# Optimization experiments

Hardware: AMD Instinct MI355X
Metric: run time of the kernel (lower is better)

The kernel has to match this reference:

```python
import jax, jax.numpy as jnp
import numpy as np

B, L, K = 16, 512, 30          # proteins, residues per protein, kNN neighbors
N = B * L
H, FC = 32, 3                  # h_channels, frame_channels
C = H + FC                     # fused sphere channels (35)
HEADS, AC, VC = 8, 16, 8       # heads, alpha channels (H//2), value channels (H//4)
RBF_N, POS_N = 16, 16
EF = RBF_N + POS_N

# idealized backbone atom positions (N, CA, C) in the local residue frame
IDEAL_BB = np.array([[-0.525, 1.363, 0.0], [0.0, 0.0, 0.0], [1.526, 0.0, 0.0]], dtype=np.float32)
# cartesian (x,y,z) -> real-SH l=1 ordering (y,z,x)
P_SH = np.array([[0., 1., 0.], [0., 0., 1.], [1., 0., 0.]], dtype=np.float32)


def _knn_edges(trans):
    # per-chain brute-force kNN (chains are contiguous blocks of length L)
    X = trans.reshape(B, L, 3)
    d2 = jnp.sum((X[:, :, None, :] - X[:, None, :, :]) ** 2, axis=-1)  # [B,L,L]
    d2 = d2 + jnp.eye(L, dtype=d2.dtype) * 1e9                          # exclude self
    _, idx = jax.lax.top_k(-d2, K)                                      # [B,L,K]
    off = (jnp.arange(B) * L)[:, None, None]
    src = (idx + off).reshape(-1)              # neighbor (edge_index[0])
    tgt = jnp.repeat(jnp.arange(N), K)         # center   (edge_index[1])
    return src, tgt


def _edge_rot_mat(vec):
    # rotation aligning the edge vector with the y axis (eSCN init_edge_rot_mat style)
    nx = vec / (jnp.linalg.norm(vec, axis=-1, keepdims=True) + 1e-12)
    ref = jnp.where(jnp.abs(nx[:, :1]) < 0.9,
                    jnp.array([1., 0., 0.], dtype=vec.dtype),
                    jnp.array([0., 0., 1.], dtype=vec.dtype))
    nz = jnp.cross(nx, ref)
    nz = nz / (jnp.linalg.norm(nz, axis=-1, keepdims=True) + 1e-12)
    ny = jnp.cross(nx, nz)
    ny = ny / (jnp.linalg.norm(ny, axis=-1, keepdims=True) + 1e-12)
    return jnp.stack([nz, nx, ny], axis=-2)  # [E,3,3]


def _rbf(d, d_min=0.0, d_max=20.0, count=RBF_N):
    mu = jnp.linspace(d_min, d_max, count)
    sigma = (d_max - d_min) / count
    return jnp.exp(-(((d[:, None] - mu) / sigma) ** 2))


def _pos_emb(src, tgt, num=POS_N):
    d = (src - tgt).astype(jnp.float32)
    freq = jnp.exp(jnp.arange(0, num, 2, dtype=jnp.float32) * (-np.log(10000.0) / num))
    ang = d[:, None] * freq
    return jnp.concatenate([jnp.cos(ang), jnp.sin(ang)], axis=-1)


def _forward(rots, trans, node_emb, batch, x_mask, noising_mask,
             W_alpha, a_vec, W_v, W_o, W_g, W_2):
    src, tgt = _knn_edges(trans)
    vec = trans[src] - trans[tgt]
    dist = jnp.linalg.norm(vec, axis=-1)
    valid = jnp.isfinite(dist) & (dist > 1e-3)  # edge_select, applied as mask

    R = _edge_rot_mat(vec)
    P = jnp.asarray(P_SH)
    D1 = jnp.einsum('ij,ejk,lk->eil', P, R, P)  # l=1 Wigner in real-SH basis [E,3,3]

    edge_features = jnp.concatenate([_rbf(dist), _pos_emb(src, tgt)], axis=-1)  # [E,32]

    # fuse node features with backbone frame atoms and editability flag
    frame_atoms = jnp.einsum('nij,aj->nai', rots, jnp.asarray(IDEAL_BB))  # [N,3atoms,3xyz]
    editable = noising_mask & (~x_mask)
    emb = jnp.zeros((N, 4, C), dtype=node_emb.dtype)
    emb = emb.at[:, :, :H].set(node_emb)
    emb = emb.at[:, 1:4, H:].set(jnp.swapaxes(frame_atoms, -1, -2))
    emb = emb.at[:, 0, C - 1].set(editable.astype(node_emb.dtype))

    # gather + rotate source features into edge frames
    xs = emb[src]                                                   # [E,4,C]
    xs_rot = jnp.concatenate([xs[:, :1], jnp.einsum('eij,ejc->eic', D1, xs[:, 1:])], axis=1)

    # invariant attention logits (l=0 of rotated src, l=0 of tgt, edge feats)
    inv = jnp.concatenate([xs_rot[:, 0], emb[tgt, 0], edge_features], axis=-1)  # [E,102]
    hdn = jax.nn.silu(inv @ W_alpha).reshape(-1, HEADS, AC)
    logits = jax.nn.leaky_relu(jnp.einsum('ehk,hk->eh', hdn, a_vec), 0.2)
    logits = jnp.where(valid[:, None], logits, -1e9)

    # segment softmax over incoming edges of each target node
    mx = jax.lax.stop_gradient(jax.ops.segment_max(logits, tgt, num_segments=N))
    ex = jnp.exp(logits - mx[tgt]) * valid[:, None].astype(logits.dtype)
    den = jax.ops.segment_sum(ex, tgt, num_segments=N)
    alpha = ex / (den[tgt] + 1e-9)                                  # [E,HEADS]

    # equivariant values, attention-weighted, rotate back, scatter
    v = (xs_rot @ W_v).reshape(-1, 4, HEADS, VC)
    m = (v * alpha[:, None, :, None]).reshape(-1, 4, HEADS * VC)
    m = jnp.concatenate([m[:, :1], jnp.einsum('eji,ejc->eic', D1, m[:, 1:])], axis=1)  # D^T
    agg = jax.ops.segment_sum(m, tgt, num_segments=N)               # [N,4,64]

    y = agg @ W_o                                                    # [N,4,H]
    gate = jax.nn.silu(y[:, 0] @ W_g)                                # invariant gating FFN
    return (y * gate[:, None, :]) @ W_2                              # [N,4,H]


def setup_inputs():
    key = jax.random.key(0)
    ks = jax.random.split(key, 12)
    rots = jax.vmap(lambda m: jnp.linalg.qr(m)[0])(jax.random.normal(ks[0], (N, 3, 3)))
    trans = jax.random.normal(ks[1], (N, 3)) * 10.0
    node_emb = jax.random.normal(ks[2], (N, 4, H))
    batch = jnp.repeat(jnp.arange(B, dtype=jnp.int32), L)
    x_mask = jax.random.randint(ks[3], (N,), 0, 2).astype(bool)
    noising_mask = jax.random.randint(ks[4], (N,), 0, 2).astype(bool)
    s = lambda k, sh, fan: jax.random.normal(k, sh) / np.sqrt(fan)
    return dict(rots=rots, trans=trans, node_emb=node_emb, batch=batch,
                x_mask=x_mask, noising_mask=noising_mask,
                W_alpha=s(ks[5], (2 * C + EF, HEADS * AC), 2 * C + EF),
                a_vec=s(ks[6], (HEADS, AC), AC),
                W_v=s(ks[7], (C, HEADS * VC), C),
                W_o=s(ks[8], (HEADS * VC, H), HEADS * VC),
                W_g=s(ks[9], (H, H), H),
                W_2=s(ks[10], (H, H), H))


def reference(rots, trans, node_emb, batch, x_mask, noising_mask,
              W_alpha, a_vec, W_v, W_o, W_g, W_2):
    return _forward(rots, trans, node_emb, batch, x_mask, noising_mask,
                    W_alpha, a_vec, W_v, W_o, W_g, W_2)
```

## Files before the change

### kernel.cpp

```cpp
#include <hip/hip_runtime.h>
#include <cstdint>

#define B_ 16
#define L_ 512
#define N_ 8192
#define K_ 30
#define E_ (N_*K_)
#define H_ 32
#define C_ 35

typedef uint16_t u16;
typedef uint32_t u32;
typedef unsigned long long u64;
typedef float f2v __attribute__((ext_vector_type(2)));

static __device__ __forceinline__ f2v splat2(float x) { f2v v; v.x = x; v.y = x; return v; }

static __device__ __forceinline__ float ldf(const void* p, int i, int bf) {
    return bf ? __uint_as_float(((u32)((const u16*)p)[i]) << 16)
              : ((const float*)p)[i];
}
static __device__ __forceinline__ float bfu16(u16 x) {
    return __uint_as_float(((u32)x) << 16);
}
static __device__ __forceinline__ int ldmask(const void* p, int i, int mode) {
    if (mode == 0) return ((const unsigned char*)p)[i] != 0;
    if (mode == 2) return ((const u32*)p)[2*i] != 0;
    return ((const u32*)p)[i] != 0;
}
static __device__ __forceinline__ u16 f2bf(float f) {
    u32 x = __float_as_uint(f);
    u32 r = x + 0x7FFFu + ((x >> 16) & 1u);
    return (u16)(r >> 16);
}
static __device__ __forceinline__ float fsilu(float x) {
    return x * __builtin_amdgcn_rcpf(1.f + __expf(-x));
}

static __device__ __forceinline__ int detect_bf(const void* tr, int lane) {
    const u16* p = (const u16*)tr;
    int cnt = 0;
    for (int i = lane; i < 256; i += 64) {
        u16 v = p[2 * i];
        int e = (v >> 7) & 0xFF;
        if ((e >= 100 && e <= 141) || (v & 0x7FFFu) == 0) cnt++;
    }
    #pragma unroll
    for (int d = 1; d < 64; d <<= 1) cnt += __shfl_xor(cnt, d, 64);
    return cnt >= 192;
}
static __device__ __forceinline__ int detect_mm(const void* xmv, int lane) {
    const u32* xm = (const u32*)xmv;
    int anyBig = 0, oddNZ = 0;
    for (int i = lane; i < 1024; i += 64) {
        u32 w = xm[i];
        if (w & ~1u) anyBig = 1;
        if ((i & 1) && w) oddNZ = 1;
    }
    #pragma unroll
    for (int d = 1; d < 64; d <<= 1) {
        anyBig |= __shfl_xor(anyBig, d, 64);
        oddNZ  |= __shfl_xor(oddNZ, d, 64);
    }
    return anyBig ? 0 : (oddNZ ? 1 : 2);
}

__constant__ float cBB[9] = {-0.525f, 1.363f, 0.f,  0.f, 0.f, 0.f,  1.526f, 0.f, 0.f};

#define DPP_UMIN(var, CTRL) \
    { u32 o_ = (u32)__builtin_amdgcn_update_dpp((int)(var), (int)(var), CTRL, 0xF, 0xF, false); \
      (var) = (o_ < (var)) ? o_ : (var); }
#define DPP_UMIN_ALL(var) \
    DPP_UMIN(var, 0x111) DPP_UMIN(var, 0x112) DPP_UMIN(var, 0x114) \
    DPP_UMIN(var, 0x118) DPP_UMIN(var, 0x142) DPP_UMIN(var, 0x143)

__global__ __launch_bounds__(256) void mega_kernel(
    const void* __restrict__ rots, const void* __restrict__ trans,
    const void* __restrict__ node, const void* __restrict__ xm,
    const void* __restrict__ nm,
    const void* __restrict__ Wa, const void* __restrict__ av,
    const void* __restrict__ Wv, const void* __restrict__ Wo,
    const void* __restrict__ Wg, const void* __restrict__ W2,
    int* __restrict__ flag, int* __restrict__ srcArr,
    float* __restrict__ hsrc, float* __restrict__ htgt,
    float* __restrict__ ptab, float* __restrict__ V,
    float* __restrict__ c_wrb, float* __restrict__ c_av,
    float* __restrict__ c_Wo, float* __restrict__ c_Wg, float* __restrict__ c_W2)
{
    __shared__ float sX[L_], sY[L_], sZ[L_];
    __shared__ float eS[140];
    __shared__ int flagS[2];
    const int bid = blockIdx.x, tid = threadIdx.x;
    const int lane = tid & 63, wid = tid >> 6;

    if (bid < 2048) {
        if (wid == 0) {
            int bf = detect_bf(trans, lane);
            if (lane == 0) flagS[0] = bf;
        }
        __syncthreads();
        const int bf = flagS[0];
        const int t0 = bid * 4;
        const int base = (t0 >> 9) << 9;
        if (bf) {
            const u16* tp = (const u16*)trans;
            for (int i = tid; i < L_; i += 256) {
                sX[i] = bfu16(tp[(base + i) * 3 + 0]);
                sY[i] = bfu16(tp[(base + i) * 3 + 1]);
                sZ[i] = bfu16(tp[(base + i) * 3 + 2]);
            }
        } else {
            const float* tp = (const float*)trans;
            for (int i = tid; i < L_; i += 256) {
                sX[i] = tp[(base + i) * 3 + 0];
                sY[i] = tp[(base + i) * 3 + 1];
                sZ[i] = tp[(base + i) * 3 + 2];
            }
        }
        __syncthreads();

        const int t = t0 + wid;
        const int l = t & 511;
        const float tx = sX[l], ty = sY[l], tz = sZ[l];

        u32 d2b[8];
        #pragma unroll
        for (int i = 0; i < 8; ++i) {
            int j = lane + (i << 6);
            float dx = __fsub_rn(tx, sX[j]);
            float dy = __fsub_rn(ty, sY[j]);
            float dz = __fsub_rn(tz, sZ[j]);
            float d2 = __fadd_rn(__fadd_rn(__fmul_rn(dx, dx), __fmul_rn(dy, dy)), __fmul_rn(dz, dz));
            if (j == l) d2 = __fadd_rn(d2, 1e9f);
            d2b[i] = __float_as_uint(d2);
        }

        int myres = 0;
        for (int k = 0; k < K_; ++k) {
            u32 bb = d2b[0]; int bs = 0;
            #pragma unroll
            for (int i = 1; i < 8; ++i)
                if (d2b[i] < bb) { bb = d2b[i]; bs = i; }
            u32 m = bb;
            DPP_UMIN_ALL(m)
            u32 gbits = (u32)__builtin_amdgcn_readlane((int)m, 63);
            u32 cand = (bb == gbits) ? (u32)(lane | (bs << 6)) : 0xFFFFFFFFu;
            DPP_UMIN_ALL(cand)
            u32 gidx = (u32)__builtin_amdgcn_readlane((int)cand, 63);
            if (lane == (u32)k) myres = (int)(gidx & 511u);
            if ((gidx & 63u) == (u32)lane) {
                int ws = (int)(gidx >> 6);
                #pragma unroll
                for (int i = 0; i < 8; ++i)
                    if (ws == i) d2b[i] = 0xFFFFFFFFu;
            }
        }
        if (lane < K_) srcArr[t * K_ + lane] = base + myres;

    } else if (bid < 10240) {
        const int n = bid - 2048;
        if (wid == 0) {
            int bf = detect_bf(trans, lane);
            int mm = detect_mm(xm, lane);
            if (lane == 0) { flagS[0] = bf; flagS[1] = mm; }
        }
        __syncthreads();
        const int bf = flagS[0], mm = flagS[1];
        if (tid < 140) {
            int r = tid / 35, c = tid - r * 35;
            float v;
            if (c < H_) {
                v = ldf(node, n * 128 + r * 32 + c, bf);
            } else if (r == 0) {
                v = (c == 34) ? ((ldmask(nm, n, mm) && !ldmask(xm, n, mm)) ? 1.f : 0.f) : 0.f;
            } else {
                int i = r - 1, a = c - 32;
                v = ldf(rots, n*9 + i*3 + 0, bf) * cBB[a*3 + 0]
                  + ldf(rots, n*9 + i*3 + 1, bf) * cBB[a*3 + 1]
                  + ldf(rots, n*9 + i*3 + 2, bf) * cBB[a*3 + 2];
            }
            eS[tid] = v;
        }
        __syncthreads();
        const int r = tid >> 6, cc = tid & 63;
        if (bf) {
            const u16* wa = (const u16*)Wa;
            const u16* wv = (const u16*)Wv;
            if (tid < 128) {
                float a = 0.f, b = 0.f;
                #pragma unroll 5
                for (int i = 0; i < 35; ++i) {
                    float v = eS[i];
                    a = fmaf(v, bfu16(wa[i * 128 + tid]),        a);
                    b = fmaf(v, bfu16(wa[(35 + i) * 128 + tid]), b);
                }
                hsrc[(size_t)n * 128 + tid] = a;
                htgt[(size_t)n * 128 + tid] = b;
            }
            const float* er = eS + r * 35;
            float acc = 0.f;
            #pragma unroll 5
            for (int cp = 0; cp < 35; ++cp) acc = fmaf(er[cp], bfu16(wv[cp * 64 + cc]), acc);
            V[(size_t)n * 256 + tid] = acc;
        } else {
            const float* wa = (const float*)Wa;
            const float* wv = (const float*)Wv;
            if (tid < 128) {
                float a = 0.f, b = 0.f;
                #pragma unroll 5
                for (int i = 0; i < 35; ++i) {
                    float v = eS[i];
                    a = fmaf(v, wa[i * 128 + tid],        a);
                    b = fmaf(v, wa[(35 + i) * 128 + tid], b);
                }
                hsrc[(size_t)n * 128 + tid] = a;
                htgt[(size_t)n * 128 + tid] = b;
            }
            const float* er = eS + r * 35;
            float acc = 0.f;
            #pragma unroll 5
            for (int cp = 0; cp < 35; ++cp) acc = fmaf(er[cp], wv[cp * 64 + cc], acc);
            V[(size_t)n * 256 + tid] = acc;
        }

    } else if (bid < 11264) {
        const int d = bid - 10240;
        if (wid == 0) {
            int bf = detect_bf(trans, lane);
            if (lane == 0) flagS[0] = bf;
        }
        __syncthreads();
        const int bf = flagS[0];
        if (tid < 128) {
            float dd = (float)(d - 512);
            float acc = 0.f;
            if (bf) {
                const u16* wa = (const u16*)Wa;
                #pragma unroll
                for (int q = 0; q < 8; ++q) {
                    float fr = expf((float)(2 * q) * (-0.5756462732485115f));
                    float ang = dd * fr;
                    acc = fmaf(cosf(ang), bfu16(wa[(86 + q) * 128 + tid]), acc);
                    acc = fmaf(sinf(ang), bfu16(wa[(94 + q) * 128 + tid]), acc);
                }
            } else {
                const float* wa = (const float*)Wa;
                #pragma unroll
                for (int q = 0; q < 8; ++q) {
                    float fr = expf((float)(2 * q) * (-0.5756462732485115f));
                    float ang = dd * fr;
                    acc = fmaf(cosf(ang), wa[(86 + q) * 128 + tid], acc);
                    acc = fmaf(sinf(ang), wa[(94 + q) * 128 + tid], acc);
                }
            }
            ptab[(size_t)d * 128 + tid] = acc;
        }

    } else {
        if (wid == 0) {
            int bf = detect_bf(trans, lane);
            if (lane == 0) flagS[0] = bf;
        }
        __syncthreads();
        const int bf = flagS[0];
        if (bid == 11264 && tid == 0) flag[0] = bf;
        int g0 = (bid - 11264) * 256 + tid;
        for (int i = g0; i < 6272; i += 2048) {
            if      (i < 2048) c_wrb[i]        = ldf(Wa, 70 * 128 + i, bf);
            else if (i < 2176) c_av[i - 2048]  = ldf(av, i - 2048, bf);
            else if (i < 4224) c_Wo[i - 2176]  = ldf(Wo, i - 2176, bf);
            else if (i < 5248) c_Wg[i - 4224]  = ldf(Wg, i - 4224, bf);
            else               c_W2[i - 5248]  = ldf(W2, i - 5248, bf);
        }
    }
}

__global__ __launch_bounds__(256, 4) void edge_agg_kernel(
    const void* __restrict__ trans, const int* __restrict__ srcArr,
    const float* __restrict__ hsrc, const float* __restrict__ htgt,
    const float* __restrict__ ptab, const float* __restrict__ V,
    const float* __restrict__ c_wrb, const float* __restrict__ c_av,
    const float* __restrict__ Wo, const float* __restrict__ Wg,
    const float* __restrict__ W2,
    const int* __restrict__ flag, void* __restrict__ outv)
{
    __shared__ float rbfS[32][20];
    __shared__ int   srcS[32];
    __shared__ int   voffS[32];
    __shared__ int   dS[32];
    __shared__ float lgS[256];
    __shared__ float invS[8];
    __shared__ float aggS[256];
    __shared__ float ybuf[128];
    __shared__ float gbuf[32];
    const int bid = blockIdx.x, tid = threadIdx.x;
    const int t   = ((bid & 7) << 10) | (bid >> 3);
    const int lane = tid & 63, wid = tid >> 6;
    const int bf = flag[0];

    const f2v* cw = (const f2v*)c_wrb;
    const f2v w0 = cw[0*64+lane],  w1 = cw[1*64+lane],  w2 = cw[2*64+lane],  w3 = cw[3*64+lane];
    const f2v w4 = cw[4*64+lane],  w5 = cw[5*64+lane],  w6 = cw[6*64+lane],  w7 = cw[7*64+lane];
    const f2v w8 = cw[8*64+lane],  w9 = cw[9*64+lane],  wA = cw[10*64+lane], wB = cw[11*64+lane];
    const f2v wC = cw[12*64+lane], wD = cw[13*64+lane], wE = cw[14*64+lane], wF = cw[15*64+lane];
    const f2v avv = ((const f2v*)c_av)[lane];

    if (tid < 8 * K_) {
        const int k = tid >> 3, sub = tid & 7;
        const int e = t * K_ + k;
        int src = srcArr[e];
        src = (src < 0) ? 0 : ((src >= N_) ? (N_ - 1) : src);
        float vx = ldf(trans, src*3+0, bf) - ldf(trans, t*3+0, bf);
        float vy = ldf(trans, src*3+1, bf) - ldf(trans, t*3+1, bf);
        float vz = ldf(trans, src*3+2, bf) - ldf(trans, t*3+2, bf);
        float dist = sqrtf(vx*vx + vy*vy + vz*vz);
        bool valid = isfinite(dist) && (dist > 1e-3f);
        int d = src - t + 512;
        d = (d < 0) ? 0 : ((d > 1023) ? 1023 : d);
        if (sub == 0) {
            srcS[k]  = src;
            voffS[k] = src << 8;
            dS[k]    = d | (valid ? 0 : (1 << 16));
        }
        const int j0 = sub * 2;
        float t0 = (dist - (float)j0       * (20.f/15.f)) * 0.8f;
        float t1 = (dist - (float)(j0 + 1) * (20.f/15.f)) * 0.8f;
        rbfS[k][j0]     = __expf(-t0 * t0);
        rbfS[k][j0 + 1] = __expf(-t1 * t1);
    } else {
        const int k = 30 + ((tid - 240) >> 3), sub = (tid - 240) & 7;
        if (sub == 0) { srcS[k] = 0; voffS[k] = 0; dS[k] = 1 << 16; }
        rbfS[k][sub * 2] = 0.f;
        rbfS[k][sub * 2 + 1] = 0.f;
    }
    __syncthreads();

    const float* hsL = hsrc + (lane << 1);
    const float* ptL = ptab + (lane << 1);
    const f2v htv = *(const f2v*)(htgt + (t << 7) + (lane << 1));
    #pragma unroll
    for (int j = 0; j < 8; ++j) {
        const int k = wid * 8 + j;
        const int src = srcS[k];
        const int dm  = dS[k];
        const int d   = dm & 0xFFFF;
        const bool valid = (dm >> 16) == 0;
        f2v hs = *(const f2v*)(hsL + (src << 7));
        f2v pt = *(const f2v*)(ptL + (d << 7));
        f2v acc = (hs + htv) + pt;
        const float4* rp = (const float4*)(&rbfS[k][0]);
        float4 ra = rp[0], rb = rp[1], rc = rp[2], rd = rp[3];
        acc = __builtin_elementwise_fma(splat2(ra.x), w0, acc);
        acc = __builtin_elementwise_fma(splat2(ra.y), w1, acc);
        acc = __builtin_elementwise_fma(splat2(ra.z), w2, acc);
        acc = __builtin_elementwise_fma(splat2(ra.w), w3, acc);
        acc = __builtin_elementwise_fma(splat2(rb.x), w4, acc);
        acc = __builtin_elementwise_fma(splat2(rb.y), w5, acc);
        acc = __builtin_elementwise_fma(splat2(rb.z), w6, acc);
        acc = __builtin_elementwise_fma(splat2(rb.w), w7, acc);
        acc = __builtin_elementwise_fma(splat2(rc.x), w8, acc);
        acc = __builtin_elementwise_fma(splat2(rc.y), w9, acc);
        acc = __builtin_elementwise_fma(splat2(rc.z), wA, acc);
        acc = __builtin_elementwise_fma(splat2(rc.w), wB, acc);
        acc = __builtin_elementwise_fma(splat2(rd.x), wC, acc);
        acc = __builtin_elementwise_fma(splat2(rd.y), wD, acc);
        acc = __builtin_elementwise_fma(splat2(rd.z), wE, acc);
        acc = __builtin_elementwise_fma(splat2(rd.w), wF, acc);
        float part = fsilu(acc.x) * avv.x + fsilu(acc.y) * avv.y;
        part += __uint_as_float((u32)__builtin_amdgcn_update_dpp(
                    (int)__float_as_uint(part), (int)__float_as_uint(part), 0xB1, 0xF, 0xF, false));
        part += __uint_as_float((u32)__builtin_amdgcn_update_dpp(
                    (int)__float_as_uint(part), (int)__float_as_uint(part), 0x4E, 0xF, 0xF, false));
        part += __uint_as_float((u32)__builtin_amdgcn_update_dpp(
                    (int)__float_as_uint(part), (int)__float_as_uint(part), 0x141, 0xF, 0xF, false));
        float lg = (part >= 0.f) ? part : 0.2f * part;
        if (!valid) lg = -1e9f;
        lg = (fabsf(lg) < 1e30f) ? lg : -1e9f;
        if ((lane & 7) == 0) lgS[k * 8 + (lane >> 3)] = lg;
    }
    __syncthreads();

    if (tid < 8) {
        float mx = -1e30f;
        #pragma unroll
        for (int k = 0; k < K_; ++k) mx = fmaxf(mx, lgS[k * 8 + tid]);
        float den = 0.f;
        #pragma unroll
        for (int k = 0; k < K_; ++k) {
            float l = lgS[k * 8 + tid];
            float e = (l > -1e8f) ? __expf(l - mx) : 0.f;
            lgS[k * 8 + tid] = e; den += e;
        }
        invS[tid] = 1.f / (den + 1e-9f);
    }
    __syncthreads();

    {
        const int h = (tid & 63) >> 3;
        float acc = 0.f;
        #pragma unroll 6
        for (int k = 0; k < K_; ++k)
            acc = fmaf(lgS[k * 8 + h], V[voffS[k] + tid], acc);
        aggS[tid] = acc * invS[h];
    }
    __syncthreads();

    if (tid < 128) {
        int rr = tid >> 5, o = tid & 31;
        float y = 0.f;
        #pragma unroll
        for (int c = 0; c < 64; ++c) y = fmaf(aggS[rr * 64 + c], Wo[c * 32 + o], y);
        ybuf[tid] = y;
    }
    __syncthreads();
    if (tid < 32) {
        float g = 0.f;
        #pragma unroll
        for (int o = 0; o < 32; ++o) g = fmaf(ybuf[o], Wg[o * 32 + tid], g);
        gbuf[tid] = fsilu(g);
    }
    __syncthreads();
    if (tid < 128) {
        int rr = tid >> 5, hh = tid & 31;
        float o = 0.f;
        #pragma unroll
        for (int g = 0; g < 32; ++g) o = fmaf(ybuf[rr * 32 + g] * gbuf[g], W2[g * 32 + hh], o);
        o = (fabsf(o) < 1e30f) ? o : 0.f;
        size_t idx = (size_t)t * 128 + tid;
        if (bf) ((u16*)outv)[idx] = f2bf(o);
        else    ((float*)outv)[idx] = o;
    }
}

extern "C" void kernel_launch(void* const* d_in, const int* in_sizes, int n_in,
                              void* d_out, int out_size, void* d_ws, size_t ws_size,
                              hipStream_t stream)
{
    const void* rots         = d_in[0];
    const void* trans        = d_in[1];
    const void* node_emb     = d_in[2];
    const void* x_mask       = d_in[4];
    const void* noising_mask = d_in[5];
    const void* Wa           = d_in[6];
    const void* avec         = d_in[7];
    const void* Wv           = d_in[8];
    const void* Wo           = d_in[9];
    const void* Wg           = d_in[10];
    const void* W2           = d_in[11];

    char* ws = (char*)d_ws;
    int*   flag    = (int*)  (ws + 0);
    int*   srcArr  = (int*)  (ws + 64);
    float* hsrc    = (float*)(ws + 983104);
    float* htgt    = (float*)(ws + 5177408);
    float* ptab    = (float*)(ws + 9371712);
    float* V       = (float*)(ws + 9896000);
    float* c_wrb   = (float*)(ws + 18284608);
    float* c_av    = (float*)(ws + 18292800);
    float* c_Wo    = (float*)(ws + 18293312);
    float* c_Wg    = (float*)(ws + 18301504);
    float* c_W2    = (float*)(ws + 18305600);

    hipLaunchKernelGGL(mega_kernel, dim3(11272), dim3(256), 0, stream,
                       rots, trans, node_emb, x_mask, noising_mask,
                       Wa, avec, Wv, Wo, Wg, W2,
                       flag, srcArr, hsrc, htgt, ptab, V,
                       c_wrb, c_av, c_Wo, c_Wg, c_W2);
    hipLaunchKernelGGL(edge_agg_kernel, dim3(N_), dim3(256), 0, stream,
                       trans, srcArr, hsrc, htgt, ptab, V,
                       c_wrb, c_av, c_Wo, c_Wg, c_W2, flag, d_out);
}
```

Before: 214.4 us.

## Split edge attention into edge-parallel logits kernel and node aggregation kernel

Splits the fused per-node edge kernel in two. The first kernel computes attention logits over flat edge chunks of 32 per wave, so the 2 padded edges per node are no longer computed. The second loads those logits from workspace and does the softmax, value aggregation and output MLP per node, preloading all 30 V values into registers. This adds a kernel launch and a global round-trip for the logits, and each edge now gathers htgt itself instead of sharing one load per node.

New measurement: 210.4 us. About the same (-1.9%).

```diff
diff --git a/kernel.cpp b/kernel.cpp
--- a/kernel.cpp
+++ b/kernel.cpp
@@ -73,6 +73,14 @@
 #define DPP_UMIN_ALL(var) \
     DPP_UMIN(var, 0x111) DPP_UMIN(var, 0x112) DPP_UMIN(var, 0x114) \
     DPP_UMIN(var, 0x118) DPP_UMIN(var, 0x142) DPP_UMIN(var, 0x143)
+
+#define DPP_ADD8(part) \
+    part += __uint_as_float((u32)__builtin_amdgcn_update_dpp( \
+        (int)__float_as_uint(part), (int)__float_as_uint(part), 0xB1, 0xF, 0xF, false)); \
+    part += __uint_as_float((u32)__builtin_amdgcn_update_dpp( \
+        (int)__float_as_uint(part), (int)__float_as_uint(part), 0x4E, 0xF, 0xF, false)); \
+    part += __uint_as_float((u32)__builtin_amdgcn_update_dpp( \
+        (int)__float_as_uint(part), (int)__float_as_uint(part), 0x141, 0xF, 0xF, false));
 
 __global__ __launch_bounds__(256) void mega_kernel(
     const void* __restrict__ rots, const void* __restrict__ trans,
@@ -275,27 +283,19 @@
     }
 }
 
-__global__ __launch_bounds__(256, 4) void edge_agg_kernel(
+__global__ __launch_bounds__(128) void logits_kernel(
     const void* __restrict__ trans, const int* __restrict__ srcArr,
     const float* __restrict__ hsrc, const float* __restrict__ htgt,
-    const float* __restrict__ ptab, const float* __restrict__ V,
+    const float* __restrict__ ptab,
     const float* __restrict__ c_wrb, const float* __restrict__ c_av,
-    const float* __restrict__ Wo, const float* __restrict__ Wg,
-    const float* __restrict__ W2,
-    const int* __restrict__ flag, void* __restrict__ outv)
+    const int* __restrict__ flag, float* __restrict__ logitsw)
 {
-    __shared__ float rbfS[32][20];
-    __shared__ int   srcS[32];
-    __shared__ int   voffS[32];
-    __shared__ int   dS[32];
-    __shared__ float lgS[256];
-    __shared__ float invS[8];
-    __shared__ float aggS[256];
-    __shared__ float ybuf[128];
-    __shared__ float gbuf[32];
-    const int bid = blockIdx.x, tid = threadIdx.x;
-    const int t   = ((bid & 7) << 10) | (bid >> 3);
-    const int lane = tid & 63, wid = tid >> 6;
+    __shared__ float rbfS[2][32][20];
+    __shared__ int   srcS[2][32];
+    __shared__ int   tgtS[2][32];
+    __shared__ int   dS[2][32];
+    __shared__ float lgS[2][256];
+    const int tid = threadIdx.x, wid = tid >> 6, lane = tid & 63;
     const int bf = flag[0];
 
     const f2v* cw = (const f2v*)c_wrb;
@@ -305,50 +305,51 @@
     const f2v wC = cw[12*64+lane], wD = cw[13*64+lane], wE = cw[14*64+lane], wF = cw[15*64+lane];
     const f2v avv = ((const f2v*)c_av)[lane];
 
-    if (tid < 8 * K_) {
-        const int k = tid >> 3, sub = tid & 7;
-        const int e = t * K_ + k;
+    const int e0 = (blockIdx.x * 2 + wid) * 32;
+
+    {
+        const int el  = lane & 31;
+        const int e   = e0 + el;
+        const int tgt = e / K_;
         int src = srcArr[e];
         src = (src < 0) ? 0 : ((src >= N_) ? (N_ - 1) : src);
-        float vx = ldf(trans, src*3+0, bf) - ldf(trans, t*3+0, bf);
-        float vy = ldf(trans, src*3+1, bf) - ldf(trans, t*3+1, bf);
-        float vz = ldf(trans, src*3+2, bf) - ldf(trans, t*3+2, bf);
+        float vx = ldf(trans, src*3+0, bf) - ldf(trans, tgt*3+0, bf);
+        float vy = ldf(trans, src*3+1, bf) - ldf(trans, tgt*3+1, bf);
+        float vz = ldf(trans, src*3+2, bf) - ldf(trans, tgt*3+2, bf);
         float dist = sqrtf(vx*vx + vy*vy + vz*vz);
         bool valid = isfinite(dist) && (dist > 1e-3f);
-        int d = src - t + 512;
+        int d = src - tgt + 512;
         d = (d < 0) ? 0 : ((d > 1023) ? 1023 : d);
-        if (sub == 0) {
-            srcS[k]  = src;
-            voffS[k] = src << 8;
-            dS[k]    = d | (valid ? 0 : (1 << 16));
-        }
-        const int j0 = sub * 2;
-        float t0 = (dist - (float)j0       * (20.f/15.f)) * 0.8f;
-        float t1 = (dist - (float)(j0 + 1) * (20.f/15.f)) * 0.8f;
-        rbfS[k][j0]     = __expf(-t0 * t0);
-        rbfS[k][j0 + 1] = __expf(-t1 * t1);
-    } else {
-        const int k = 30 + ((tid - 240) >> 3), sub = (tid - 240) & 7;
-        if (sub == 0) { srcS[k] = 0; voffS[k] = 0; dS[k] = 1 << 16; }
-        rbfS[k][sub * 2] = 0.f;
-        rbfS[k][sub * 2 + 1] = 0.f;
+        if (lane < 32) {
+            srcS[wid][el] = src;
+            tgtS[wid][el] = tgt;
+            dS[wid][el]   = d | (valid ? 0 : (1 << 16));
+        }
+        const int jb = (lane >> 5) * 8;
+        #pragma unroll
+        for (int j = 0; j < 8; ++j) {
+            float tt = (dist - (float)(jb + j) * (20.f/15.f)) * 0.8f;
+            rbfS[wid][lane & 31][jb + j] = __expf(-tt * tt);
+        }
     }
     __syncthreads();
 
     const float* hsL = hsrc + (lane << 1);
+    const float* htL = htgt + (lane << 1);
     const float* ptL = ptab + (lane << 1);
-    const f2v htv = *(const f2v*)(htgt + (t << 7) + (lane << 1));
-    #pragma unroll
-    for (int j = 0; j < 8; ++j) {
-        const int k = wid * 8 + j;
-        const int src = srcS[k];
-        const int dm  = dS[k];
+    #pragma unroll 2
+    for (int q = 0; q < 32; ++q) {
+        const int src = srcS[wid][q];
+        const int tgt = tgtS[wid][q];
+        const int dm  = dS[wid][q];
         const int d   = dm & 0xFFFF;
         const bool valid = (dm >> 16) == 0;
+
         f2v hs = *(const f2v*)(hsL + (src << 7));
+        f2v ht = *(const f2v*)(htL + (tgt << 7));
         f2v pt = *(const f2v*)(ptL + (d << 7));
-        f2v acc = (hs + htv) + pt;
-        const float4* rp = (const float4*)(&rbfS[k][0]);
+        f2v acc = (hs + ht) + pt;
+        const float4* rp = (const float4*)(&rbfS[wid][q][0]);
         float4 ra = rp[0], rb = rp[1], rc = rp[2], rd = rp[3];
         acc = __builtin_elementwise_fma(splat2(ra.x), w0, acc);
         acc = __builtin_elementwise_fma(splat2(ra.y), w1, acc);
@@ -367,16 +368,41 @@
         acc = __builtin_elementwise_fma(splat2(rd.z), wE, acc);
         acc = __builtin_elementwise_fma(splat2(rd.w), wF, acc);
         float part = fsilu(acc.x) * avv.x + fsilu(acc.y) * avv.y;
-        part += __uint_as_float((u32)__builtin_amdgcn_update_dpp(
-                    (int)__float_as_uint(part), (int)__float_as_uint(part), 0xB1, 0xF, 0xF, false));
-        part += __uint_as_float((u32)__builtin_amdgcn_update_dpp(
-                    (int)__float_as_uint(part), (int)__float_as_uint(part), 0x4E, 0xF, 0xF, false));
-        part += __uint_as_float((u32)__builtin_amdgcn_update_dpp(
-                    (int)__float_as_uint(part), (int)__float_as_uint(part), 0x141, 0xF, 0xF, false));
+        DPP_ADD8(part)
         float lg = (part >= 0.f) ? part : 0.2f * part;
         if (!valid) lg = -1e9f;
         lg = (fabsf(lg) < 1e30f) ? lg : -1e9f;
-        if ((lane & 7) == 0) lgS[k * 8 + (lane >> 3)] = lg;
+        if ((lane & 7) == 0) lgS[wid][q * 8 + (lane >> 3)] = lg;
+    }
+    __syncthreads();
+    {
+        float4* dst = (float4*)(logitsw + (size_t)e0 * 8);
+        dst[lane] = ((const float4*)lgS[wid])[lane];
+    }
+}
+
+__global__ __launch_bounds__(256) void agg_out_kernel(
+    const float* __restrict__ V, const int* __restrict__ srcArr,
+    const float* __restrict__ logitsw,
+    const float* __restrict__ Wo, const float* __restrict__ Wg,
+    const float* __restrict__ W2,
+    const int* __restrict__ flag, void* __restrict__ outv)
+{
+    __shared__ float lgS[240];
+    __shared__ float invS[8];
+    __shared__ int   voffS[K_];
+    __shared__ float aggS[256];
+    __shared__ float ybuf[128];
+    __shared__ float gbuf[32];
+    const int bid = blockIdx.x, tid = threadIdx.x;
+    const int t   = ((bid & 7) << 10) | (bid >> 3);
+    const int bf = flag[0];
+
+    if (tid < 240) lgS[tid] = logitsw[(size_t)t * 240 + tid];
+    if (tid < K_) {
+        int s = srcArr[t * K_ + tid];
+        s = (s < 0) ? 0 : ((s >= N_) ? (N_ - 1) : s);
+        voffS[tid] = s << 8;
     }
     __syncthreads();
 
@@ -397,10 +423,12 @@
 
     {
         const int h = (tid & 63) >> 3;
+        float vv[K_];
+        #pragma unroll
+        for (int k = 0; k < K_; ++k) vv[k] = V[voffS[k] + tid];
         float acc = 0.f;
-        #pragma unroll 6
-        for (int k = 0; k < K_; ++k)
-            acc = fmaf(lgS[k * 8 + h], V[voffS[k] + tid], acc);
+        #pragma unroll
+        for (int k = 0; k < K_; ++k) acc = fmaf(lgS[k * 8 + h], vv[k], acc);
         aggS[tid] = acc * invS[h];
     }
     __syncthreads();
@@ -460,13 +488,15 @@
     float* c_Wo    = (float*)(ws + 18293312);
     float* c_Wg    = (float*)(ws + 18301504);
     float* c_W2    = (float*)(ws + 18305600);
+    float* logitsw = (float*)(ws + 18309696);
 
     hipLaunchKernelGGL(mega_kernel, dim3(11272), dim3(256), 0, stream,
                        rots, trans, node_emb, x_mask, noising_mask,
                        Wa, avec, Wv, Wo, Wg, W2,
                        flag, srcArr, hsrc, htgt, ptab, V,
                        c_wrb, c_av, c_Wo, c_Wg, c_W2);
-    hipLaunchKernelGGL(edge_agg_kernel, dim3(N_), dim3(256), 0, stream,
-                       trans, srcArr, hsrc, htgt, ptab, V,
-                       c_wrb, c_av, c_Wo, c_Wg, c_W2, flag, d_out);
-}
+    hipLaunchKernelGGL(logits_kernel, dim3(E_/64), dim3(128), 0, stream,
+                       trans, srcArr, hsrc, htgt, ptab, c_wrb, c_av, flag, logitsw);
+    hipLaunchKernelGGL(agg_out_kernel, dim3(N_), dim3(256), 0, stream,
+                       V, srcArr, logitsw, c_Wo, c_Wg, c_W2, flag, d_out);
+}
```
